# Optimization experiments

Measured on AMD Instinct MI355X. Metric: run time of the kernel, lower is better.

The kernel has to match this reference:

```python
import jax, jax.numpy as jnp
import numpy as np
from jax import lax

NUM_GROUP = 512
GROUP_SIZE = 32


def setup_inputs() -> dict:
    key = jax.random.key(0)
    xyz = jax.random.normal(key, (8, 8192, 6), dtype=jnp.float32)
    return {"xyz": xyz}


def _fps_indices(pts, K):
    """Farthest point sampling. pts: [B,N,3] -> idx [B,K] int32. Start at point 0."""
    B, N, _ = pts.shape
    first = jnp.zeros((B,), dtype=jnp.int32)
    # squared distance of every point to the first selected point
    d = jnp.sum((pts - pts[:, :1, :]) ** 2, axis=-1)  # [B,N]

    def step(d, _):
        nxt = jnp.argmax(d, axis=1).astype(jnp.int32)              # [B]
        newp = jnp.take_along_axis(pts, nxt[:, None, None], axis=1)  # [B,1,3]
        d = jnp.minimum(d, jnp.sum((pts - newp) ** 2, axis=-1))
        return d, nxt

    _, rest = lax.scan(step, d, None, length=K - 1)  # rest: [K-1,B]
    idx = jnp.concatenate([first[None, :], rest], axis=0)  # [K,B]
    return idx.T  # [B,K]


def _group(xyz, num_group, group_size):
    coords = xyz[:, :, :3]    # [B,N,3]
    normals = xyz[:, :, 3:6]  # [B,N,3]

    fps_idx = _fps_indices(coords, num_group)                          # [B,G]
    center = jnp.take_along_axis(coords, fps_idx[:, :, None], axis=1)  # [B,G,3]

    # pairwise squared distances center->points: [B,G,N]
    c2 = jnp.sum(center ** 2, axis=-1)[:, :, None]
    x2 = jnp.sum(coords ** 2, axis=-1)[:, None, :]
    cx = jnp.einsum('bgd,bnd->bgn', center, coords)
    d2 = c2 - 2.0 * cx + x2

    _, knn_idx = lax.top_k(-d2, group_size)  # [B,G,M] nearest neighbors

    flat_idx = knn_idx.reshape(knn_idx.shape[0], -1)  # [B,G*M]
    neigh = jnp.take_along_axis(coords, flat_idx[:, :, None], axis=1)
    neigh = neigh.reshape(-1, num_group, group_size, 3) - center[:, :, None, :]
    neigh_n = jnp.take_along_axis(normals, flat_idx[:, :, None], axis=1)
    neigh_n = neigh_n.reshape(-1, num_group, group_size, 3)
    return neigh, neigh_n, center


def reference(xyz):
    return _group(xyz, NUM_GROUP, GROUP_SIZE)
```

## Files before the change

### kernel.cpp

```cpp
#include <hip/hip_runtime.h>
#include <stdint.h>

#define BATCH 8
#define NPTS 8192
#define NGRP 512
#define GSZ 32

typedef float vf2 __attribute__((ext_vector_type(2)));

__device__ __forceinline__ float sq3(float dx, float dy, float dz) {
    return __fadd_rn(__fadd_rn(__fmul_rn(dx, dx), __fmul_rn(dy, dy)), __fmul_rn(dz, dz));
}

template <int C>
__device__ __forceinline__ float dpp_max_f32_step(float v) {
    const int t = __builtin_amdgcn_update_dpp(__float_as_int(v), __float_as_int(v),
                                              C, 0xF, 0xF, false);
    return fmaxf(v, __int_as_float(t));
}
template <int C>
__device__ __forceinline__ unsigned dpp_min_u32_step(unsigned v) {
    const unsigned t = (unsigned)__builtin_amdgcn_update_dpp((int)v, (int)v,
                                                             C, 0xF, 0xF, false);
    return v < t ? v : t;
}
__device__ __forceinline__ float wave_max_f32(float v) {
    v = dpp_max_f32_step<0x111>(v);
    v = dpp_max_f32_step<0x112>(v);
    v = dpp_max_f32_step<0x114>(v);
    v = dpp_max_f32_step<0x118>(v);
    v = dpp_max_f32_step<0x142>(v);
    v = dpp_max_f32_step<0x143>(v);
    return __int_as_float(__builtin_amdgcn_readlane(__float_as_int(v), 63));
}
__device__ __forceinline__ unsigned wave_min_u32(unsigned v) {
    v = dpp_min_u32_step<0x111>(v);
    v = dpp_min_u32_step<0x112>(v);
    v = dpp_min_u32_step<0x114>(v);
    v = dpp_min_u32_step<0x118>(v);
    v = dpp_min_u32_step<0x142>(v);
    v = dpp_min_u32_step<0x143>(v);
    return (unsigned)__builtin_amdgcn_readlane((int)v, 63);
}

__global__ __launch_bounds__(512) void fps_kernel(const float* __restrict__ xyz,
                                                  float* __restrict__ centers) {
    const int b = blockIdx.x;
    const int tid = threadIdx.x;
    const int lane = tid & 63;
    const int wv = tid >> 6;

    __shared__ float4 P4[NPTS];
    __shared__ double pkey[2][8];
    __shared__ float cl[NGRP * 3];

    vf2 px[8], py[8], pz[8], d2[8];
    const float* base = xyz + (size_t)b * NPTS * 6;

#pragma unroll
    for (int i = 0; i < 16; ++i) {
        const int p = i * 512 + tid;
        const float* q = base + (size_t)p * 6;
        const float x = q[0], y = q[1], z = q[2];
        px[i >> 1][i & 1] = x; py[i >> 1][i & 1] = y; pz[i >> 1][i & 1] = z;
        d2[i >> 1][i & 1] = __int_as_float(0x7f800000);
        P4[p] = make_float4(x, y, z, 0.0f);
    }
    float Bx = base[0], By = base[1], Bz = base[2];
    if (tid == 0) { cl[0] = Bx; cl[1] = By; cl[2] = Bz; }
    __syncthreads();

    for (int k = 1; k < NGRP; ++k) {
        {
#pragma clang fp contract(off)
            const vf2 bx2 = {Bx, Bx}, by2 = {By, By}, bz2 = {Bz, Bz};
#pragma unroll
            for (int j = 0; j < 8; ++j) {
                const vf2 dx = px[j] - bx2;
                const vf2 dy = py[j] - by2;
                const vf2 dz = pz[j] - bz2;
                const vf2 mx2 = dx * dx;
                const vf2 my2 = dy * dy;
                const vf2 mz2 = dz * dz;
                const vf2 s = (mx2 + my2) + mz2;
                d2[j] = __builtin_elementwise_min(d2[j], s);
            }
        }
        vf2 mv = d2[0];
#pragma unroll
        for (int j = 1; j < 8; ++j) mv = __builtin_elementwise_max(mv, d2[j]);
        const float mx = fmaxf(mv[0], mv[1]);
        const float wmx = wave_max_f32(mx);
        int wi = 0;
#pragma unroll
        for (int i = 15; i >= 1; --i) {
            wi = (d2[i >> 1][i & 1] == mx) ? i : wi;
        }
        const unsigned cand = (mx == wmx) ? (unsigned)(wi * 512 + tid) : 0xFFFFFFFFu;
        const unsigned widx_w = wave_min_u32(cand);

        const int buf = k & 1;
        if (lane == 0) {
            pkey[buf][wv] =
                __hiloint2double(__float_as_int(wmx), 8191 - (int)widx_w);
        }
        __syncthreads();

        double g = pkey[buf][0];
#pragma unroll
        for (int w = 1; w < 8; ++w) g = fmax(g, pkey[buf][w]);
        const int widx = 8191 - __double2loint(g);
        const float4 c4 = P4[widx];
        Bx = c4.x; By = c4.y; Bz = c4.z;

        if (tid == 0) { cl[k * 3 + 0] = Bx; cl[k * 3 + 1] = By; cl[k * 3 + 2] = Bz; }
    }

    __syncthreads();
    float* cg = centers + (size_t)b * NGRP * 3;
    for (int t = tid; t < NGRP * 3; t += 512) cg[t] = cl[t];
}

__global__ __launch_bounds__(256) void knn_kernel(const float* __restrict__ xyz,
                                                  const float* __restrict__ centers,
                                                  float* __restrict__ neigh,
                                                  float* __restrict__ neigh_n) {
    const int row = blockIdx.x;
    const int b = row >> 9;
    const int tid = threadIdx.x;
    const int lane = tid & 63;
    const int wv = tid >> 6;

    __shared__ unsigned long long rk[2][4];
    __shared__ int sel[GSZ];

    const float* cptr = centers + (size_t)row * 3;
    const float cx = cptr[0], cy = cptr[1], cz = cptr[2];
    const float c2 = sq3(cx, cy, cz);

    const float* base = xyz + (size_t)b * NPTS * 6;
    unsigned long long key[32];
#pragma unroll
    for (int i = 0; i < 32; ++i) {
        const int p = i * 256 + tid;
        const float* q = base + (size_t)p * 6;
        const float x = q[0], y = q[1], z = q[2];
        const float x2 = sq3(x, y, z);
        const float dot = __fmaf_rn(cz, z, __fmaf_rn(cy, y, __fmul_rn(cx, x)));
        const float d2 = __fadd_rn(__fsub_rn(c2, __fmul_rn(2.0f, dot)), x2);
        unsigned u = __float_as_uint(d2);
        u = (u & 0x80000000u) ? ~u : (u | 0x80000000u);
        key[i] = ((unsigned long long)u << 32) | (unsigned)p;
    }

    unsigned long long lm = key[0];
#pragma unroll
    for (int i = 1; i < 32; ++i) lm = key[i] < lm ? key[i] : lm;

    for (int r = 0; r < GSZ; ++r) {
        const unsigned hi = (unsigned)(lm >> 32);
        const unsigned minhi = wave_min_u32(hi);
        const unsigned cand = (hi == minhi) ? (unsigned)lm : 0xFFFFFFFFu;
        const unsigned minlo = wave_min_u32(cand);
        const unsigned long long mk = ((unsigned long long)minhi << 32) | minlo;

        const int rb = r & 1;
        if (lane == 0) rk[rb][wv] = mk;
        __syncthreads();
        const unsigned long long g01 = rk[rb][0] < rk[rb][1] ? rk[rb][0] : rk[rb][1];
        const unsigned long long g23 = rk[rb][2] < rk[rb][3] ? rk[rb][2] : rk[rb][3];
        const unsigned long long gm = g01 < g23 ? g01 : g23;
        if (tid == 0) sel[r] = (int)(unsigned)(gm & 0xffffffffu);
        if (lm == gm) {
#pragma unroll
            for (int i = 0; i < 32; ++i) {
                if (key[i] == gm) key[i] = ~0ULL;
            }
            lm = key[0];
#pragma unroll
            for (int i = 1; i < 32; ++i) lm = key[i] < lm ? key[i] : lm;
        }
    }
    __syncthreads();

    if (tid < GSZ) {
        const int idx = sel[tid];
        const float* q = base + (size_t)idx * 6;
        const size_t o = ((size_t)row * GSZ + tid) * 3;
        neigh[o + 0] = __fsub_rn(q[0], cx);
        neigh[o + 1] = __fsub_rn(q[1], cy);
        neigh[o + 2] = __fsub_rn(q[2], cz);
        neigh_n[o + 0] = q[3];
        neigh_n[o + 1] = q[4];
        neigh_n[o + 2] = q[5];
    }
}

extern "C" void kernel_launch(void* const* d_in, const int* in_sizes, int n_in,
                              void* d_out, int out_size, void* d_ws, size_t ws_size,
                              hipStream_t stream) {
    const float* xyz = (const float*)d_in[0];
    float* out = (float*)d_out;
    float* neigh   = out;
    float* neigh_n = out + (size_t)BATCH * NGRP * GSZ * 3;
    float* centers = out + (size_t)2 * BATCH * NGRP * GSZ * 3;

    fps_kernel<<<BATCH, 512, 0, stream>>>(xyz, centers);
    knn_kernel<<<BATCH * NGRP, 256, 0, stream>>>(xyz, centers, neigh, neigh_n);
}
```

Before: 629.3 us.

## Add ballot fast paths, second-min caching, and vectorized loads to FPS and KNN

FPS and KNN now check with a ballot whether exactly one lane holds the wave extreme. If so, they read that lane's index directly instead of running a second DPP min reduction. KNN keeps a cached second-smallest key per thread, so after a pick it can skip one of the 32-key rescans, and later rescans use a threshold instead of overwriting keys. Point loads become float4/float2 vector loads, which are misaligned for odd point indices because of the 24-byte stride. The LDS reductions also use wider reads. This trims per-iteration reduction and rescan work, at the cost of divergent branches and reliance on unaligned global vector loads.

```diff
diff --git a/kernel.cpp b/kernel.cpp
--- a/kernel.cpp
+++ b/kernel.cpp
@@ -47,7 +47,6 @@
                                                   float* __restrict__ centers) {
     const int b = blockIdx.x;
     const int tid = threadIdx.x;
-    const int lane = tid & 63;
     const int wv = tid >> 6;
 
     __shared__ float4 P4[NPTS];
@@ -60,11 +59,10 @@
 #pragma unroll
     for (int i = 0; i < 16; ++i) {
         const int p = i * 512 + tid;
-        const float* q = base + (size_t)p * 6;
-        const float x = q[0], y = q[1], z = q[2];
-        px[i >> 1][i & 1] = x; py[i >> 1][i & 1] = y; pz[i >> 1][i & 1] = z;
+        const float4 v4 = *reinterpret_cast<const float4*>(base + (size_t)p * 6);
+        px[i >> 1][i & 1] = v4.x; py[i >> 1][i & 1] = v4.y; pz[i >> 1][i & 1] = v4.z;
         d2[i >> 1][i & 1] = __int_as_float(0x7f800000);
-        P4[p] = make_float4(x, y, z, 0.0f);
+        P4[p] = make_float4(v4.x, v4.y, v4.z, 0.0f);
     }
     float Bx = base[0], By = base[1], Bz = base[2];
     if (tid == 0) { cl[0] = Bx; cl[1] = By; cl[2] = Bz; }
@@ -96,19 +94,26 @@
         for (int i = 15; i >= 1; --i) {
             wi = (d2[i >> 1][i & 1] == mx) ? i : wi;
         }
-        const unsigned cand = (mx == wmx) ? (unsigned)(wi * 512 + tid) : 0xFFFFFFFFu;
-        const unsigned widx_w = wave_min_u32(cand);
+        unsigned widx_w;
+        const unsigned long long bal = __ballot(mx == wmx);
+        if (__popcll(bal) == 1) {
+            const int L = __ffsll(bal) - 1;
+            widx_w = (unsigned)(__builtin_amdgcn_readlane(wi, L) * 512 + (wv * 64 + L));
+        } else {
+            const unsigned cand = (mx == wmx) ? (unsigned)(wi * 512 + tid) : 0xFFFFFFFFu;
+            widx_w = wave_min_u32(cand);
+        }
 
         const int buf = k & 1;
-        if (lane == 0) {
-            pkey[buf][wv] =
-                __hiloint2double(__float_as_int(wmx), 8191 - (int)widx_w);
+        if ((tid & 63) == 0) {
+            pkey[buf][wv] = __hiloint2double(__float_as_int(wmx), 8191 - (int)widx_w);
         }
         __syncthreads();
 
-        double g = pkey[buf][0];
-#pragma unroll
-        for (int w = 1; w < 8; ++w) g = fmax(g, pkey[buf][w]);
+        const double2* pp = reinterpret_cast<const double2*>(&pkey[buf][0]);
+        const double2 a = pp[0], c = pp[1], e = pp[2], f = pp[3];
+        const double g = fmax(fmax(fmax(a.x, a.y), fmax(c.x, c.y)),
+                              fmax(fmax(e.x, e.y), fmax(f.x, f.y)));
         const int widx = 8191 - __double2loint(g);
         const float4 c4 = P4[widx];
         Bx = c4.x; By = c4.y; Bz = c4.z;
@@ -143,42 +148,62 @@
 #pragma unroll
     for (int i = 0; i < 32; ++i) {
         const int p = i * 256 + tid;
-        const float* q = base + (size_t)p * 6;
-        const float x = q[0], y = q[1], z = q[2];
+        const float4 v4 = *reinterpret_cast<const float4*>(base + (size_t)p * 6);
+        const float x = v4.x, y = v4.y, z = v4.z;
         const float x2 = sq3(x, y, z);
         const float dot = __fmaf_rn(cz, z, __fmaf_rn(cy, y, __fmul_rn(cx, x)));
         const float d2 = __fadd_rn(__fsub_rn(c2, __fmul_rn(2.0f, dot)), x2);
         unsigned u = __float_as_uint(d2);
-        u = (u & 0x80000000u) ? ~u : (u | 0x80000000u);
+        u ^= (unsigned)(((int)u >> 31)) | 0x80000000u;
         key[i] = ((unsigned long long)u << 32) | (unsigned)p;
     }
 
-    unsigned long long lm = key[0];
-#pragma unroll
-    for (int i = 1; i < 32; ++i) lm = key[i] < lm ? key[i] : lm;
+    unsigned long long lm = ~0ULL, lm2v = ~0ULL;
+#pragma unroll
+    for (int i = 0; i < 32; ++i) {
+        const unsigned long long kk = key[i];
+        const bool a = kk < lm;
+        const bool b2 = kk < lm2v;
+        lm2v = a ? lm : (b2 ? kk : lm2v);
+        lm = a ? kk : lm;
+    }
 
     for (int r = 0; r < GSZ; ++r) {
         const unsigned hi = (unsigned)(lm >> 32);
         const unsigned minhi = wave_min_u32(hi);
-        const unsigned cand = (hi == minhi) ? (unsigned)lm : 0xFFFFFFFFu;
-        const unsigned minlo = wave_min_u32(cand);
+        unsigned minlo;
+        const unsigned long long bal = __ballot(hi == minhi);
+        if (__popcll(bal) == 1) {
+            const int L = __ffsll(bal) - 1;
+            minlo = (unsigned)__builtin_amdgcn_readlane((int)(unsigned)lm, L);
+        } else {
+            const unsigned cand = (hi == minhi) ? (unsigned)lm : 0xFFFFFFFFu;
+            minlo = wave_min_u32(cand);
+        }
         const unsigned long long mk = ((unsigned long long)minhi << 32) | minlo;
 
         const int rb = r & 1;
         if (lane == 0) rk[rb][wv] = mk;
         __syncthreads();
-        const unsigned long long g01 = rk[rb][0] < rk[rb][1] ? rk[rb][0] : rk[rb][1];
-        const unsigned long long g23 = rk[rb][2] < rk[rb][3] ? rk[rb][2] : rk[rb][3];
+        const ulonglong2* rp = reinterpret_cast<const ulonglong2*>(&rk[rb][0]);
+        const ulonglong2 r0 = rp[0], r1 = rp[1];
+        const unsigned long long g01 = r0.x < r0.y ? r0.x : r0.y;
+        const unsigned long long g23 = r1.x < r1.y ? r1.x : r1.y;
         const unsigned long long gm = g01 < g23 ? g01 : g23;
         if (tid == 0) sel[r] = (int)(unsigned)(gm & 0xffffffffu);
         if (lm == gm) {
-#pragma unroll
-            for (int i = 0; i < 32; ++i) {
-                if (key[i] == gm) key[i] = ~0ULL;
+            if (lm2v != 0ULL) {
+                lm = lm2v;
+            } else {
+                unsigned long long nm = ~0ULL;
+#pragma unroll
+                for (int i = 0; i < 32; ++i) {
+                    const unsigned long long v = key[i] > gm ? key[i] : ~0ULL;
+                    nm = v < nm ? v : nm;
+                }
+                lm = nm;
             }
-            lm = key[0];
-#pragma unroll
-            for (int i = 1; i < 32; ++i) lm = key[i] < lm ? key[i] : lm;
+            lm2v = 0ULL;
         }
     }
     __syncthreads();
@@ -186,13 +211,15 @@
     if (tid < GSZ) {
         const int idx = sel[tid];
         const float* q = base + (size_t)idx * 6;
+        const float4 a4 = *reinterpret_cast<const float4*>(q);
+        const float2 b2v = *reinterpret_cast<const float2*>(q + 4);
         const size_t o = ((size_t)row * GSZ + tid) * 3;
-        neigh[o + 0] = __fsub_rn(q[0], cx);
-        neigh[o + 1] = __fsub_rn(q[1], cy);
-        neigh[o + 2] = __fsub_rn(q[2], cz);
-        neigh_n[o + 0] = q[3];
-        neigh_n[o + 1] = q[4];
-        neigh_n[o + 2] = q[5];
+        neigh[o + 0] = __fsub_rn(a4.x, cx);
+        neigh[o + 1] = __fsub_rn(a4.y, cy);
+        neigh[o + 2] = __fsub_rn(a4.z, cz);
+        neigh_n[o + 0] = a4.w;
+        neigh_n[o + 1] = b2v.x;
+        neigh_n[o + 2] = b2v.y;
     }
 }
 
```

Result: faster. 511.9 us (median of 3 runs) (-18.6%).
